# Kernel optimization log

Measured on AMD Instinct MI355X. Metric: run time of the kernel, lower is better.

## Reference

```python
import jax, jax.numpy as jnp
import numpy as np
from jax import lax

H = 32  # hidden_dim

def _lstm_layer(x_tbd, W_ih, W_hh, b_ih, b_hh):
    """x_tbd: [T, B, D]. Returns all hidden states [T, B, H]. PyTorch gate order i,f,g,o."""
    T, B, _ = x_tbd.shape
    # Precompute input contribution for all timesteps (one big GEMM)
    xW = jnp.einsum('tbd,gd->tbg', x_tbd, W_ih) + (b_ih + b_hh)  # [T, B, 4H]
    W_hh_T = W_hh.T  # [H, 4H]

    def step(carry, xw):
        h, c = carry
        gates = xw + h @ W_hh_T  # [B, 4H]
        i, f, g, o = jnp.split(gates, 4, axis=-1)
        i = jax.nn.sigmoid(i)
        f = jax.nn.sigmoid(f)
        g = jnp.tanh(g)
        o = jax.nn.sigmoid(o)
        c = f * c + i * g
        h = o * jnp.tanh(c)
        return (h, c), h

    h0 = jnp.zeros((B, H), x_tbd.dtype)
    (_, _), hs = lax.scan(step, (h0, h0), xW)
    return hs  # [T, B, H]


def setup_inputs() -> dict:
    key = jax.random.key(0)
    ks = jax.random.split(key, 12)
    s = 0.1  # keep gates out of saturation
    return {
        'x': jax.random.normal(ks[0], (4096, 512, 4), jnp.float32),
        'W_ih0': jax.random.normal(ks[1], (4 * H, 4), jnp.float32) * s,
        'W_hh0': jax.random.normal(ks[2], (4 * H, H), jnp.float32) * s,
        'b_ih0': jax.random.normal(ks[3], (4 * H,), jnp.float32) * s,
        'b_hh0': jax.random.normal(ks[4], (4 * H,), jnp.float32) * s,
        'W_ih1': jax.random.normal(ks[5], (4 * H, H), jnp.float32) * s,
        'W_hh1': jax.random.normal(ks[6], (4 * H, H), jnp.float32) * s,
        'b_ih1': jax.random.normal(ks[7], (4 * H,), jnp.float32) * s,
        'b_hh1': jax.random.normal(ks[8], (4 * H,), jnp.float32) * s,
        'W_out': jax.random.normal(ks[9], (1, H), jnp.float32) * s,
        'b_out': jax.random.normal(ks[10], (1,), jnp.float32) * s,
    }


def reference(x, W_ih0, W_hh0, b_ih0, b_hh0, W_ih1, W_hh1, b_ih1, b_hh1, W_out, b_out):
    # x: [B, T, D] (batch_first). Eval mode -> inter-layer dropout is identity.
    x_tbd = jnp.transpose(x, (1, 0, 2))  # [T, B, D]
    h1 = _lstm_layer(x_tbd, W_ih0, W_hh0, b_ih0, b_hh0)  # [T, B, H]
    h2 = _lstm_layer(h1, W_ih1, W_hh1, b_ih1, b_hh1)     # [T, B, H]
    last = h2[-1]  # [B, H] == out[:, -1, :]
    return last @ W_out.T + b_out  # [B, 1]
```

## Files before the change

### kernel.cpp

```cpp
#include <hip/hip_runtime.h>
#include <cmath>

constexpr int T   = 512;
constexpr int D   = 4;
constexpr int H   = 32;
constexpr int BT  = 16;
constexpr int BLK = 256;

constexpr float LOG2E     = 1.44269504088896340736f;
constexpr float NEG2LOG2E = -2.88539008177792681472f;

constexpr int XSTRIDE = 4104;
constexpr int HSTR = 40;

typedef short bf8 __attribute__((ext_vector_type(8)));
typedef float f4  __attribute__((ext_vector_type(4)));
typedef float f2  __attribute__((ext_vector_type(2)));

static __device__ __forceinline__ short bf16_rtn(float v) {
    unsigned u = __float_as_uint(v);
    u += 0x7FFFu + ((u >> 16) & 1u);
    return (short)(u >> 16);
}

__global__ __launch_bounds__(BLK, 1) void lstm_bf16p(
    const float* __restrict__ x,
    const float* __restrict__ W_ih0, const float* __restrict__ W_hh0,
    const float* __restrict__ b_ih0, const float* __restrict__ b_hh0,
    const float* __restrict__ W_ih1, const float* __restrict__ W_hh1,
    const float* __restrict__ b_ih1, const float* __restrict__ b_hh1,
    const float* __restrict__ W_out, const float* __restrict__ b_out,
    float* __restrict__ out)
{
    __shared__ __align__(16) short xbf[16 * XSTRIDE];
    __shared__ __align__(16) short h0b[2][16][HSTR];
    __shared__ __align__(16) short h1b[2][16][HSTR];
    __shared__ __align__(16) float h1f[16][36];

    const int tid   = threadIdx.x;
    const int w     = tid >> 6;
    const int lane  = tid & 63;
    const int q     = lane >> 4;
    const int nl    = lane & 15;
    const int layer = w >> 1;
    const int ug    = (w & 1) << 4;
    const int b0    = blockIdx.x * BT;

    for (int idx = tid; idx < 16 * T; idx += BLK) {
        const int col = idx & 15;
        const int t   = idx >> 4;
        float4 xv = *(const float4*)(x + ((size_t)(b0 + col) * T + t) * D);
        bf8 v = {0, 0, 0, 0, 0, 0, 0, 0};
        v[0] = bf16_rtn(xv.x); v[1] = bf16_rtn(xv.y);
        v[2] = bf16_rtn(xv.z); v[3] = bf16_rtn(xv.w);
        *(bf8*)&xbf[col * XSTRIDE + t * 8] = v;
    }
    for (int idx = tid; idx < 2 * 16 * HSTR; idx += BLK) {
        (&h0b[0][0][0])[idx] = 0;
        (&h1b[0][0][0])[idx] = 0;
    }

    const float* W1 = layer ? W_ih1 : W_hh0;
    bf8 w1[4], w2[4];
    f4  bias[4];
    #pragma unroll
    for (int g = 0; g < 4; ++g) {
        const float sc = (g == 2) ? NEG2LOG2E : -LOG2E;
        const int row = 32 * g + ug + nl;
        #pragma unroll
        for (int j = 0; j < 8; ++j) {
            w1[g][j] = bf16_rtn(W1[row * H + 8 * q + j] * sc);
            float v2 = layer ? W_hh1[row * H + 8 * q + j]
                             : ((q == 0 && j < 4) ? W_ih0[row * D + j] : 0.0f);
            w2[g][j] = bf16_rtn(v2 * sc);
        }
        #pragma unroll
        for (int r = 0; r < 4; ++r) {
            const int gr = 32 * g + ug + 4 * q + r;
            bias[g][r] = sc * (layer ? (b_ih1[gr] + b_hh1[gr])
                                     : (b_ih0[gr] + b_hh0[gr]));
        }
    }

    f4 c4 = {0.0f, 0.0f, 0.0f, 0.0f};

    const short* xcol = &xbf[nl * XSTRIDE];

    __syncthreads();

    auto actquad = [&](const f4 zi, const f4 zf, const f4 zg, const f4 zo,
                       unsigned& pk0, unsigned& pk1, f4& hv) {
        f4 ei, ef, eg, eo, ec;
        #pragma unroll
        for (int e = 0; e < 4; ++e) {
            ei[e] = __builtin_amdgcn_exp2f(zi[e]);
            ef[e] = __builtin_amdgcn_exp2f(zf[e]);
            eg[e] = __builtin_amdgcn_exp2f(zg[e]);
            eo[e] = __builtin_amdgcn_exp2f(zo[e]);
        }
        f4 D1 = 1.0f + ef;
        f4 D2 = (1.0f + ei) * (1.0f + eg);
        f4 Dm = D1 * D2;
        float s0 = Dm[0] * Dm[1], s1 = Dm[2] * Dm[3];
        float R  = __builtin_amdgcn_rcpf(s0 * s1);
        float t0 = R * s1, t1 = R * s0;
        f4 inv;
        inv[0] = t0 * Dm[1]; inv[1] = t0 * Dm[0];
        inv[2] = t1 * Dm[3]; inv[3] = t1 * Dm[2];
        c4 = (c4 * D2 + (1.0f - eg) * D1) * inv;
        #pragma unroll
        for (int e = 0; e < 4; ++e)
            ec[e] = __builtin_amdgcn_exp2f(c4[e] * NEG2LOG2E);
        f4 Do = (1.0f + eo) * (1.0f + ec);
        float u0 = Do[0] * Do[1], u1 = Do[2] * Do[3];
        float Q  = __builtin_amdgcn_rcpf(u0 * u1);
        float v0 = Q * u1, v1 = Q * u0;
        f4 invo;
        invo[0] = v0 * Do[1]; invo[1] = v0 * Do[0];
        invo[2] = v1 * Do[3]; invo[3] = v1 * Do[2];
        hv = (1.0f - ec) * invo;
        asm("v_cvt_pk_bf16_f32 %0, %1, %2" : "=v"(pk0) : "v"(hv[0]), "v"(hv[1]));
        asm("v_cvt_pk_bf16_f32 %0, %1, %2" : "=v"(pk1) : "v"(hv[2]), "v"(hv[3]));
    };

    auto body = [&](const int i, const int rb, const int wb) {
        bf8 b2;
        if (layer == 0) {
            b2 = *(const bf8*)&xcol[(i & (T - 1)) * 8];
        } else {
            b2 = *(const bf8*)&h1b[rb][nl][8 * q];
        }
        bf8 b1 = *(const bf8*)&h0b[rb][nl][8 * q];

        f4 acc[4];
        #pragma unroll
        for (int g = 0; g < 4; ++g) {
            f4 A = __builtin_amdgcn_mfma_f32_16x16x32_bf16(w2[g], b2, bias[g], 0, 0, 0);
            A    = __builtin_amdgcn_mfma_f32_16x16x32_bf16(w1[g], b1, A,       0, 0, 0);
            acc[g] = A;
        }

        const bool act = layer ? (i >= 1) : (i < T);
        if (act) {
            unsigned pk0, pk1;
            f4 hv;
            actquad(acc[0], acc[1], acc[2], acc[3], pk0, pk1, hv);
            int2 hh; hh.x = (int)pk0; hh.y = (int)pk1;
            if (layer == 0) {
                *(int2*)&h0b[wb][nl][ug + 4 * q] = hh;
            } else {
                *(int2*)&h1b[wb][nl][ug + 4 * q] = hh;
                if (i == T) {
                    float4 hw;
                    hw.x = hv[0]; hw.y = hv[1]; hw.z = hv[2]; hw.w = hv[3];
                    *(float4*)&h1f[nl][ug + 4 * q] = hw;
                }
            }
        }
        __syncthreads();
    };

    #pragma unroll 1
    for (int i = 0; i < T; i += 2) {
        body(i,     0, 1);
        body(i + 1, 1, 0);
    }
    body(T, 0, 1);

    if (tid < BT) {
        float acc = b_out[0];
        #pragma unroll
        for (int u = 0; u < H; ++u) acc = fmaf(W_out[u], h1f[tid][u], acc);
        out[b0 + tid] = acc;
    }
}

extern "C" void kernel_launch(void* const* d_in, const int* in_sizes, int n_in,
                              void* d_out, int out_size, void* d_ws, size_t ws_size,
                              hipStream_t stream) {
    const float* x     = (const float*)d_in[0];
    const float* W_ih0 = (const float*)d_in[1];
    const float* W_hh0 = (const float*)d_in[2];
    const float* b_ih0 = (const float*)d_in[3];
    const float* b_hh0 = (const float*)d_in[4];
    const float* W_ih1 = (const float*)d_in[5];
    const float* W_hh1 = (const float*)d_in[6];
    const float* b_ih1 = (const float*)d_in[7];
    const float* b_hh1 = (const float*)d_in[8];
    const float* W_out = (const float*)d_in[9];
    const float* b_out = (const float*)d_in[10];
    float* out = (float*)d_out;

    const int B = out_size;
    lstm_bf16p<<<B / BT, BLK, 0, stream>>>(x, W_ih0, W_hh0, b_ih0, b_hh0,
                                           W_ih1, W_hh1, b_ih1, b_hh1,
                                           W_out, b_out, out);
}
```

Baseline: 279.9 us.

## Give each LSTM layer one wave and pipeline layers via lagged ring buffer

Each layer now runs on a single wavefront that computes all 32 hidden units for its 16 batch columns, so the per-step hidden state stays in registers instead of being exchanged through shared memory. Layer 1 consumes layer-0 outputs from a 16-slot ring buffer lagged by 8 steps, so the block synchronises once per 8 timesteps instead of every step. The cost is twice the MFMA and activation work per wave and only two waves per block, which may expose the latency of the serial dependency chain.

```diff
diff --git a/kernel.cpp b/kernel.cpp
--- a/kernel.cpp
+++ b/kernel.cpp
@@ -5,17 +5,18 @@
 constexpr int D   = 4;
 constexpr int H   = 32;
 constexpr int BT  = 16;
-constexpr int BLK = 256;
+constexpr int BLK = 128;
+constexpr int LAG = 8;
+constexpr int NS  = 16;
 
 constexpr float LOG2E     = 1.44269504088896340736f;
 constexpr float NEG2LOG2E = -2.88539008177792681472f;
 
 constexpr int XSTRIDE = 4104;
-constexpr int HSTR = 40;
+constexpr int RSTR = 36;
 
 typedef short bf8 __attribute__((ext_vector_type(8)));
 typedef float f4  __attribute__((ext_vector_type(4)));
-typedef float f2  __attribute__((ext_vector_type(2)));
 
 static __device__ __forceinline__ short bf16_rtn(float v) {
     unsigned u = __float_as_uint(v);
@@ -23,7 +24,7 @@
     return (short)(u >> 16);
 }
 
-__global__ __launch_bounds__(BLK, 1) void lstm_bf16p(
+__global__ __launch_bounds__(BLK, 1) void lstm_pi(
     const float* __restrict__ x,
     const float* __restrict__ W_ih0, const float* __restrict__ W_hh0,
     const float* __restrict__ b_ih0, const float* __restrict__ b_hh0,
@@ -33,18 +34,15 @@
     float* __restrict__ out)
 {
     __shared__ __align__(16) short xbf[16 * XSTRIDE];
-    __shared__ __align__(16) short h0b[2][16][HSTR];
-    __shared__ __align__(16) short h1b[2][16][HSTR];
+    __shared__ __align__(16) short h0r[NS][16][RSTR];
     __shared__ __align__(16) float h1f[16][36];
 
-    const int tid   = threadIdx.x;
-    const int w     = tid >> 6;
-    const int lane  = tid & 63;
-    const int q     = lane >> 4;
-    const int nl    = lane & 15;
-    const int layer = w >> 1;
-    const int ug    = (w & 1) << 4;
-    const int b0    = blockIdx.x * BT;
+    const int tid  = threadIdx.x;
+    const int isL0 = (tid < 64);
+    const int lane = tid & 63;
+    const int q    = lane >> 4;
+    const int nl   = lane & 15;
+    const int b0   = blockIdx.x * BT;
 
     for (int idx = tid; idx < 16 * T; idx += BLK) {
         const int col = idx & 15;
@@ -55,40 +53,45 @@
         v[2] = bf16_rtn(xv.z); v[3] = bf16_rtn(xv.w);
         *(bf8*)&xbf[col * XSTRIDE + t * 8] = v;
     }
-    for (int idx = tid; idx < 2 * 16 * HSTR; idx += BLK) {
-        (&h0b[0][0][0])[idx] = 0;
-        (&h1b[0][0][0])[idx] = 0;
-    }
-
-    const float* W1 = layer ? W_ih1 : W_hh0;
-    bf8 w1[4], w2[4];
-    f4  bias[4];
+
+    const float* W1 = isL0 ? W_hh0 : W_ih1;
+    bf8 w1[4][2], w2[4][2];
+    f4  bias[4][2];
     #pragma unroll
     for (int g = 0; g < 4; ++g) {
         const float sc = (g == 2) ? NEG2LOG2E : -LOG2E;
-        const int row = 32 * g + ug + nl;
-        #pragma unroll
-        for (int j = 0; j < 8; ++j) {
-            w1[g][j] = bf16_rtn(W1[row * H + 8 * q + j] * sc);
-            float v2 = layer ? W_hh1[row * H + 8 * q + j]
-                             : ((q == 0 && j < 4) ? W_ih0[row * D + j] : 0.0f);
-            w2[g][j] = bf16_rtn(v2 * sc);
-        }
-        #pragma unroll
-        for (int r = 0; r < 4; ++r) {
-            const int gr = 32 * g + ug + 4 * q + r;
-            bias[g][r] = sc * (layer ? (b_ih1[gr] + b_hh1[gr])
-                                     : (b_ih0[gr] + b_hh0[gr]));
+        #pragma unroll
+        for (int hf = 0; hf < 2; ++hf) {
+            const int row = 32 * g + 16 * hf + nl;
+            #pragma unroll
+            for (int j = 0; j < 8; ++j) {
+                const int kk = (j < 4) ? (4 * q + j) : (16 + 4 * q + (j - 4));
+                w1[g][hf][j] = bf16_rtn(W1[row * H + kk] * sc);
+                float v2 = isL0 ? ((q == 0 && j < 4) ? W_ih0[row * D + j] : 0.0f)
+                                : W_hh1[row * H + kk];
+                w2[g][hf][j] = bf16_rtn(v2 * sc);
+            }
+            #pragma unroll
+            for (int r = 0; r < 4; ++r) {
+                const int gr = 32 * g + 16 * hf + 4 * q + r;
+                bias[g][hf][r] = sc * (isL0 ? (b_ih0[gr] + b_hh0[gr])
+                                            : (b_ih1[gr] + b_hh1[gr]));
+            }
         }
     }
 
-    f4 c4 = {0.0f, 0.0f, 0.0f, 0.0f};
+    f4 cs0 = {0.0f, 0.0f, 0.0f, 0.0f};
+    f4 cs1 = {0.0f, 0.0f, 0.0f, 0.0f};
+    bf8 hreg = {0, 0, 0, 0, 0, 0, 0, 0};
 
     const short* xcol = &xbf[nl * XSTRIDE];
 
     __syncthreads();
 
-    auto actquad = [&](const f4 zi, const f4 zf, const f4 zg, const f4 zo,
+    bf8 bx = *(const bf8*)&xcol[0];
+    bf8 rb1;
+
+    auto actquad = [&](f4& c4, const f4 zi, const f4 zf, const f4 zg, const f4 zo,
                        unsigned& pk0, unsigned& pk1, f4& hv) {
         f4 ei, ef, eg, eo, ec;
         #pragma unroll
@@ -123,49 +126,62 @@
         asm("v_cvt_pk_bf16_f32 %0, %1, %2" : "=v"(pk1) : "v"(hv[2]), "v"(hv[3]));
     };
 
-    auto body = [&](const int i, const int rb, const int wb) {
-        bf8 b2;
-        if (layer == 0) {
-            b2 = *(const bf8*)&xcol[(i & (T - 1)) * 8];
-        } else {
-            b2 = *(const bf8*)&h1b[rb][nl][8 * q];
-        }
-        bf8 b1 = *(const bf8*)&h0b[rb][nl][8 * q];
-
-        f4 acc[4];
-        #pragma unroll
-        for (int g = 0; g < 4; ++g) {
-            f4 A = __builtin_amdgcn_mfma_f32_16x16x32_bf16(w2[g], b2, bias[g], 0, 0, 0);
-            A    = __builtin_amdgcn_mfma_f32_16x16x32_bf16(w1[g], b1, A,       0, 0, 0);
-            acc[g] = A;
-        }
-
-        const bool act = layer ? (i >= 1) : (i < T);
-        if (act) {
-            unsigned pk0, pk1;
-            f4 hv;
-            actquad(acc[0], acc[1], acc[2], acc[3], pk0, pk1, hv);
-            int2 hh; hh.x = (int)pk0; hh.y = (int)pk1;
-            if (layer == 0) {
-                *(int2*)&h0b[wb][nl][ug + 4 * q] = hh;
-            } else {
-                *(int2*)&h1b[wb][nl][ug + 4 * q] = hh;
-                if (i == T) {
-                    float4 hw;
-                    hw.x = hv[0]; hw.y = hv[1]; hw.z = hv[2]; hw.w = hv[3];
-                    *(float4*)&h1f[nl][ug + 4 * q] = hw;
+    auto group8 = [&](const int t0, const int sbase, const bool do0, const bool do1) {
+        if (do0 && isL0) {
+            #pragma unroll
+            for (int u = 0; u < 8; ++u) {
+                bf8 b2 = bx;
+                bx = *(const bf8*)&xcol[((t0 + u + 1) & (T - 1)) * 8];
+                f4 acc[4][2];
+                #pragma unroll
+                for (int g = 0; g < 4; ++g)
+                    #pragma unroll
+                    for (int hf = 0; hf < 2; ++hf) {
+                        f4 A = __builtin_amdgcn_mfma_f32_16x16x32_bf16(w2[g][hf], b2, bias[g][hf], 0, 0, 0);
+                        acc[g][hf] = __builtin_amdgcn_mfma_f32_16x16x32_bf16(w1[g][hf], hreg, A, 0, 0, 0);
+                    }
+                unsigned pka, pkb, pkc, pkd; f4 hv;
+                actquad(cs0, acc[0][0], acc[1][0], acc[2][0], acc[3][0], pka, pkb, hv);
+                actquad(cs1, acc[0][1], acc[1][1], acc[2][1], acc[3][1], pkc, pkd, hv);
+                int4 pkv; pkv.x = (int)pka; pkv.y = (int)pkb; pkv.z = (int)pkc; pkv.w = (int)pkd;
+                hreg = __builtin_bit_cast(bf8, pkv);
+                *(bf8*)&h0r[sbase + u][nl][8 * q] = hreg;
+            }
+        }
+        if (do1 && !isL0) {
+            rb1 = *(const bf8*)&h0r[(sbase + 8) & (NS - 1)][nl][8 * q];
+            #pragma unroll
+            for (int u = 0; u < 8; ++u) {
+                bf8 b1 = rb1;
+                if (u < 7)
+                    rb1 = *(const bf8*)&h0r[(sbase + u + 9) & (NS - 1)][nl][8 * q];
+                f4 acc[4][2];
+                #pragma unroll
+                for (int g = 0; g < 4; ++g)
+                    #pragma unroll
+                    for (int hf = 0; hf < 2; ++hf) {
+                        f4 A = __builtin_amdgcn_mfma_f32_16x16x32_bf16(w2[g][hf], hreg, bias[g][hf], 0, 0, 0);
+                        acc[g][hf] = __builtin_amdgcn_mfma_f32_16x16x32_bf16(w1[g][hf], b1, A, 0, 0, 0);
+                    }
+                unsigned pka, pkb, pkc, pkd; f4 hv0, hv1;
+                actquad(cs0, acc[0][0], acc[1][0], acc[2][0], acc[3][0], pka, pkb, hv0);
+                actquad(cs1, acc[0][1], acc[1][1], acc[2][1], acc[3][1], pkc, pkd, hv1);
+                int4 pkv; pkv.x = (int)pka; pkv.y = (int)pkb; pkv.z = (int)pkc; pkv.w = (int)pkd;
+                hreg = __builtin_bit_cast(bf8, pkv);
+                if (t0 + u - LAG == T - 1) {
+                    *(f4*)&h1f[nl][4 * q]      = hv0;
+                    *(f4*)&h1f[nl][16 + 4 * q] = hv1;
                 }
             }
         }
         __syncthreads();
     };
 
+    group8(0, 0, true, false);
     #pragma unroll 1
-    for (int i = 0; i < T; i += 2) {
-        body(i,     0, 1);
-        body(i + 1, 1, 0);
-    }
-    body(T, 0, 1);
+    for (int g = 1; g < 64; ++g)
+        group8(8 * g, (g & 1) * 8, true, true);
+    group8(T, 0, false, true);
 
     if (tid < BT) {
         float acc = b_out[0];
@@ -192,7 +208,7 @@
     float* out = (float*)d_out;
 
     const int B = out_size;
-    lstm_bf16p<<<B / BT, BLK, 0, stream>>>(x, W_ih0, W_hh0, b_ih0, b_hh0,
-                                           W_ih1, W_hh1, b_ih1, b_hh1,
-                                           W_out, b_out, out);
+    lstm_pi<<<B / BT, BLK, 0, stream>>>(x, W_ih0, W_hh0, b_ih0, b_hh0,
+                                        W_ih1, W_hh1, b_ih1, b_hh1,
+                                        W_out, b_out, out);
 }
```

Result: slower. 392.6 us (+40.3%).
